# Kernel optimization log

Hardware: AMD Instinct MI355X
Metric: run time of the kernel (lower is better)

## Reference

```python
import jax, jax.numpy as jnp
import numpy as np

N, DIM = 4096, 1024

def setup_inputs() -> dict:
    key = jax.random.key(0)
    ks = jax.random.split(key, 5)
    scale = 1.0 / np.sqrt(DIM)
    return {
        "x": jax.random.normal(ks[0], (N, DIM), dtype=jnp.float32),
        "Wq": jax.random.normal(ks[1], (DIM, DIM), dtype=jnp.float32) * scale,
        "bq": jax.random.normal(ks[2], (DIM,), dtype=jnp.float32) * 0.01,
        "Wk": jax.random.normal(ks[3], (DIM, DIM), dtype=jnp.float32) * scale,
        "bk": jax.random.normal(ks[4], (DIM,), dtype=jnp.float32) * 0.01,
    }

def reference(x, Wq, bq, Wk, bk):
    # torch nn.Linear: y = x @ W.T + b
    q = x @ Wq.T + bq            # [N, D]
    k = x @ Wk.T + bk            # [N, D]
    scores = q @ k.T             # [N, N] (no 1/sqrt(d) scaling, as in source)
    attn = jax.nn.softmax(scores, axis=-1)
    return attn @ x              # weighted pooling over raw x (no value proj)
```

## Files before the change

### kernel.cpp

```cpp
#include <hip/hip_runtime.h>
#include <hip/hip_bf16.h>
#include <hip/hip_fp16.h>
#include <stdint.h>


using half8   = __attribute__((ext_vector_type(8))) _Float16;
using float4v = __attribute__((ext_vector_type(4))) float;
using int4v   = __attribute__((ext_vector_type(4))) int;

#define QS        (6.0f / 32768.0f)
#define INV_S     (32768.0f / 6.0f)
#define INV_S256  (128.0f / 6.0f)
#define C_HH      (65536.0f * QS * QS)
#define C_X       (256.0f * QS * QS)

#define SX        (6.0f / 32768.0f)
#define SW        (0.25f / 32768.0f)
#define P_HH      (65536.0f * SX * SW)
#define P_X       (256.0f * SX * SW)

#define GLOAD_LDS16(gptr, ldsptr)                                              \
  __builtin_amdgcn_global_load_lds(                                            \
      (__attribute__((address_space(1))) void*)(uintptr_t)(gptr),              \
      (__attribute__((address_space(3))) void*)(unsigned)(uintptr_t)(ldsptr),  \
      16, 0, 0)

__global__ __launch_bounds__(256, 2) void gemm_s_stats(
    const int8_t* __restrict__ Ahi, const int8_t* __restrict__ Alo,
    const int8_t* __restrict__ Bhi, const int8_t* __restrict__ Blo,
    _Float16* __restrict__ E, float2* __restrict__ stats)
{
  __shared__ __align__(16) int8_t sAh[128 * 64];
  __shared__ __align__(16) int8_t sAl[128 * 64];
  __shared__ __align__(16) int8_t sBh[128 * 64];
  __shared__ __align__(16) int8_t sBl[128 * 64];

  const int tid  = threadIdx.x;
  const int wave = tid >> 6;
  const int lane = tid & 63;
  const int quad = lane >> 4;
  const int t16  = lane & 15;
  const int wm   = wave & 1;
  const int wn   = wave >> 1;
  const int row0 = blockIdx.y * 128;
  const int col0 = blockIdx.x * 128;

  const int seg  = lane & 3;
  const int rsub = lane >> 2;

  int4v hh[4][4], cc[4][4];
#pragma unroll
  for (int i = 0; i < 4; ++i)
#pragma unroll
    for (int j = 0; j < 4; ++j) {
      hh[i][j] = (int4v){0, 0, 0, 0};
      cc[i][j] = (int4v){0, 0, 0, 0};
    }

  for (int k0 = 0; k0 < 1024; k0 += 64) {
#pragma unroll
    for (int r = 0; r < 2; ++r) {
      const int trow = r * 64 + wave * 16;
      const size_t goffA = (size_t)(row0 + trow + rsub) * 2048 + k0 + seg * 16;
      const size_t goffB = (size_t)(col0 + trow + rsub) * 2048 + k0 + seg * 16;
      GLOAD_LDS16(Ahi + goffA, &sAh[trow * 64]);
      GLOAD_LDS16(Alo + goffA, &sAl[trow * 64]);
      GLOAD_LDS16(Bhi + goffB, &sBh[trow * 64]);
      GLOAD_LDS16(Blo + goffB, &sBl[trow * 64]);
    }
    __syncthreads();

    int4v ah[4], al[4], bh[4], bl[4];
#pragma unroll
    for (int i = 0; i < 4; ++i) {
      const int ar = (wm * 64 + i * 16 + t16) * 64 + quad * 16;
      ah[i] = *(const int4v*)&sAh[ar];
      al[i] = *(const int4v*)&sAl[ar];
    }
#pragma unroll
    for (int j = 0; j < 4; ++j) {
      const int br = (wn * 64 + j * 16 + t16) * 64 + quad * 16;
      bh[j] = *(const int4v*)&sBh[br];
      bl[j] = *(const int4v*)&sBl[br];
    }

#pragma unroll
    for (int i = 0; i < 4; ++i)
#pragma unroll
      for (int j = 0; j < 4; ++j) {
        hh[i][j] = __builtin_amdgcn_mfma_i32_16x16x64_i8(ah[i], bh[j], hh[i][j], 0, 0, 0);
        cc[i][j] = __builtin_amdgcn_mfma_i32_16x16x64_i8(ah[i], bl[j], cc[i][j], 0, 0, 0);
        cc[i][j] = __builtin_amdgcn_mfma_i32_16x16x64_i8(al[i], bh[j], cc[i][j], 0, 0, 0);
      }
    __syncthreads();
  }

  float* red = (float*)sAh;

  float vv[4][4][4];
  float rmax[4][4];
#pragma unroll
  for (int i = 0; i < 4; ++i)
#pragma unroll
    for (int r = 0; r < 4; ++r) {
      float mx = -3.0e38f;
#pragma unroll
      for (int j = 0; j < 4; ++j) {
        float v = C_HH * (float)hh[i][j][r] + C_X * (float)cc[i][j][r];
        vv[i][j][r] = v;
        mx = fmaxf(mx, v);
      }
      mx = fmaxf(mx, __shfl_xor(mx, 1));
      mx = fmaxf(mx, __shfl_xor(mx, 2));
      mx = fmaxf(mx, __shfl_xor(mx, 4));
      mx = fmaxf(mx, __shfl_xor(mx, 8));
      rmax[i][r] = mx;
    }
  if (t16 == 0) {
#pragma unroll
    for (int i = 0; i < 4; ++i)
#pragma unroll
      for (int r = 0; r < 4; ++r)
        red[wn * 128 + wm * 64 + i * 16 + quad * 4 + r] = rmax[i][r];
  }
  __syncthreads();

  float mrow[4][4];
#pragma unroll
  for (int i = 0; i < 4; ++i)
#pragma unroll
    for (int r = 0; r < 4; ++r) {
      const int row = wm * 64 + i * 16 + quad * 4 + r;
      mrow[i][r] = fmaxf(red[row], red[128 + row]);
    }

  float rsum[4][4];
#pragma unroll
  for (int i = 0; i < 4; ++i)
#pragma unroll
    for (int r = 0; r < 4; ++r) {
      float s = 0.f;
#pragma unroll
      for (int j = 0; j < 4; ++j) {
        float e = __expf(vv[i][j][r] - mrow[i][r]);
        vv[i][j][r] = e;
        s += e;
      }
      s += __shfl_xor(s, 1);
      s += __shfl_xor(s, 2);
      s += __shfl_xor(s, 4);
      s += __shfl_xor(s, 8);
      rsum[i][r] = s;
    }
  if (t16 == 0) {
#pragma unroll
    for (int i = 0; i < 4; ++i)
#pragma unroll
      for (int r = 0; r < 4; ++r)
        red[256 + wn * 128 + wm * 64 + i * 16 + quad * 4 + r] = rsum[i][r];
  }
  __syncthreads();

#pragma unroll
  for (int i = 0; i < 4; ++i) {
#pragma unroll
    for (int j = 0; j < 4; ++j) {
#pragma unroll
      for (int r = 0; r < 4; ++r) {
        const int crow = row0 + wm * 64 + i * 16 + quad * 4 + r;
        const int ccol = col0 + wn * 64 + j * 16 + t16;
        E[(size_t)crow * 4096 + ccol] = (_Float16)vv[i][j][r];
      }
    }
  }
  if (wn == 0 && t16 == 0) {
#pragma unroll
    for (int i = 0; i < 4; ++i)
#pragma unroll
      for (int r = 0; r < 4; ++r) {
        const int row = wm * 64 + i * 16 + quad * 4 + r;
        const float l = red[256 + row] + red[256 + 128 + row];
        stats[(size_t)(row0 + row) * 32 + blockIdx.x] =
            make_float2(mrow[i][r], l);
      }
  }
}

__global__ __launch_bounds__(256, 2) void gemm_proj_i8(
    const int8_t* __restrict__ Ahi, const int8_t* __restrict__ Alo,
    const int8_t* __restrict__ Bhi, const int8_t* __restrict__ Blo,
    const float* __restrict__ biasQ, const float* __restrict__ biasK,
    int8_t* __restrict__ Ch, int8_t* __restrict__ Cl)
{
  __shared__ __align__(16) int8_t sAh[128 * 64];
  __shared__ __align__(16) int8_t sAl[128 * 64];
  __shared__ __align__(16) int8_t sBh[128 * 64];
  __shared__ __align__(16) int8_t sBl[128 * 64];

  const int tid  = threadIdx.x;
  const int wave = tid >> 6;
  const int lane = tid & 63;
  const int quad = lane >> 4;
  const int t16  = lane & 15;
  const int wm   = wave & 1;
  const int wn   = wave >> 1;
  const int row0 = blockIdx.y * 128;
  const int col0 = blockIdx.x * 128;

  const int seg  = lane & 3;
  const int rsub = lane >> 2;

  int4v hh[4][4], cc[4][4];
#pragma unroll
  for (int i = 0; i < 4; ++i)
#pragma unroll
    for (int j = 0; j < 4; ++j) {
      hh[i][j] = (int4v){0, 0, 0, 0};
      cc[i][j] = (int4v){0, 0, 0, 0};
    }

  for (int k0 = 0; k0 < 1024; k0 += 64) {
#pragma unroll
    for (int r = 0; r < 2; ++r) {
      const int trow = r * 64 + wave * 16;
      const size_t goffA = (size_t)(row0 + trow + rsub) * 1024 + k0 + seg * 16;
      const size_t goffB = (size_t)(col0 + trow + rsub) * 1024 + k0 + seg * 16;
      GLOAD_LDS16(Ahi + goffA, &sAh[trow * 64]);
      GLOAD_LDS16(Alo + goffA, &sAl[trow * 64]);
      GLOAD_LDS16(Bhi + goffB, &sBh[trow * 64]);
      GLOAD_LDS16(Blo + goffB, &sBl[trow * 64]);
    }
    __syncthreads();

    int4v ah[4], al[4], bh[4], bl[4];
#pragma unroll
    for (int i = 0; i < 4; ++i) {
      const int ar = (wm * 64 + i * 16 + t16) * 64 + quad * 16;
      ah[i] = *(const int4v*)&sAh[ar];
      al[i] = *(const int4v*)&sAl[ar];
    }
#pragma unroll
    for (int j = 0; j < 4; ++j) {
      const int br = (wn * 64 + j * 16 + t16) * 64 + quad * 16;
      bh[j] = *(const int4v*)&sBh[br];
      bl[j] = *(const int4v*)&sBl[br];
    }

#pragma unroll
    for (int i = 0; i < 4; ++i)
#pragma unroll
      for (int j = 0; j < 4; ++j) {
        hh[i][j] = __builtin_amdgcn_mfma_i32_16x16x64_i8(ah[i], bh[j], hh[i][j], 0, 0, 0);
        cc[i][j] = __builtin_amdgcn_mfma_i32_16x16x64_i8(ah[i], bl[j], cc[i][j], 0, 0, 0);
        cc[i][j] = __builtin_amdgcn_mfma_i32_16x16x64_i8(al[i], bh[j], cc[i][j], 0, 0, 0);
      }
    __syncthreads();
  }

#pragma unroll
  for (int i = 0; i < 4; ++i) {
#pragma unroll
    for (int j = 0; j < 4; ++j) {
      const int ccol = col0 + wn * 64 + j * 16 + t16;
      const float* bp = (ccol < 1024) ? biasQ : (biasK - 1024);
#pragma unroll
      for (int r = 0; r < 4; ++r) {
        const int crow = row0 + wm * 64 + i * 16 + quad * 4 + r;
        float v = P_HH * (float)hh[i][j][r] + P_X * (float)cc[i][j][r] + bp[ccol];
        int hi = (int)lrintf(v * INV_S256);
        hi = hi > 127 ? 127 : (hi < -127 ? -127 : hi);
        int lo = (int)lrintf(v * INV_S - 256.0f * (float)hi);
        lo = lo > 127 ? 127 : (lo < -127 ? -127 : lo);
        Ch[(size_t)crow * 2048 + ccol] = (int8_t)hi;
        Cl[(size_t)crow * 2048 + ccol] = (int8_t)lo;
      }
    }
  }
}

__global__ __launch_bounds__(512) void gemm_av(
    const uint16_t* __restrict__ E, const uint16_t* __restrict__ B,
    const float2* __restrict__ stats, float* __restrict__ out)
{
  __shared__ __align__(16) uint16_t stage[16384];
  __shared__ float betaS[128 * 33];

  const int L      = blockIdx.x;
  const int xcd    = L & 7;
  const int rest   = L >> 3;
  const int colb   = rest & 7;
  const int bandHi = rest >> 3;
  const int band   = xcd + 8 * bandHi;
  const int row0   = band * 128;
  const int col0   = colb * 128;

  const int tid  = threadIdx.x;
  const int wave = tid >> 6;
  const int z    = wave >> 2;
  const int gw   = wave & 3;
  const int lane = tid & 63;
  const int quad = lane >> 4;
  const int t16  = lane & 15;
  const int wm   = gw & 1;
  const int wn   = gw >> 1;
  const int seg  = lane & 3;
  const int rsub = lane >> 2;

  if (tid < 128) {
    const int row = row0 + tid;
    float2 st[32];
    float m = -3.0e38f;
#pragma unroll
    for (int t = 0; t < 32; ++t) {
      st[t] = stats[(size_t)row * 32 + t];
      m = fmaxf(m, st[t].x);
    }
    float l = 0.f;
#pragma unroll
    for (int t = 0; t < 32; ++t) l += st[t].y * __expf(st[t].x - m);
    const float inv = 1.0f / l;
#pragma unroll
    for (int t = 0; t < 32; ++t)
      betaS[tid * 33 + t] = __expf(st[t].x - m) * inv;
  }
  __syncthreads();

  uint16_t* sA = &stage[z * 8192];
  uint16_t* sB = &stage[z * 8192 + 4096];

  float4v acc[4][4];
#pragma unroll
  for (int i = 0; i < 4; ++i)
#pragma unroll
    for (int j = 0; j < 4; ++j)
      acc[i][j] = (float4v){0.f, 0.f, 0.f, 0.f};

  for (int tt = 0; tt < 16; ++tt) {
    const int t = z * 16 + tt;
    _Float16 bb[4];
#pragma unroll
    for (int i = 0; i < 4; ++i)
      bb[i] = (_Float16)betaS[(wm * 64 + i * 16 + t16) * 33 + t];

#pragma unroll
    for (int kk = 0; kk < 4; ++kk) {
      const int k0 = t * 128 + kk * 32;
#pragma unroll
      for (int r = 0; r < 2; ++r) {
        const int trow = r * 64 + gw * 16;
        const size_t goffA = (size_t)(row0 + trow + rsub) * 4096 + k0 + seg * 8;
        const size_t goffB = (size_t)(col0 + trow + rsub) * 4096 + k0 + seg * 8;
        GLOAD_LDS16(E + goffA, &sA[trow * 32]);
        GLOAD_LDS16(B + goffB, &sB[trow * 32]);
      }
      __syncthreads();

      half8 af[4], bf[4];
#pragma unroll
      for (int i = 0; i < 4; ++i) {
        af[i] = *(const half8*)&sA[(wm * 64 + i * 16 + t16) * 32 + quad * 8];
        half8 bs;
#pragma unroll
        for (int c = 0; c < 8; ++c) bs[c] = bb[i];
        af[i] = af[i] * bs;
      }
#pragma unroll
      for (int j = 0; j < 4; ++j)
        bf[j] = *(const half8*)&sB[(wn * 64 + j * 16 + t16) * 32 + quad * 8];

#pragma unroll
      for (int i = 0; i < 4; ++i)
#pragma unroll
        for (int j = 0; j < 4; ++j)
          acc[i][j] = __builtin_amdgcn_mfma_f32_16x16x32_f16(af[i], bf[j], acc[i][j], 0, 0, 0);
      __syncthreads();
    }
  }

  float* xfer = (float*)stage;
#pragma unroll
  for (int h = 0; h < 2; ++h) {
    if (z == 1) {
#pragma unroll
      for (int i = 2 * h; i < 2 * h + 2; ++i)
#pragma unroll
        for (int j = 0; j < 4; ++j)
#pragma unroll
          for (int r = 0; r < 4; ++r) {
            const int e = (i - 2 * h) * 16 + j * 4 + r;
            xfer[e * 256 + gw * 64 + lane] = acc[i][j][r];
          }
    }
    __syncthreads();
    if (z == 0) {
#pragma unroll
      for (int i = 2 * h; i < 2 * h + 2; ++i)
#pragma unroll
        for (int j = 0; j < 4; ++j)
#pragma unroll
          for (int r = 0; r < 4; ++r) {
            const int e = (i - 2 * h) * 16 + j * 4 + r;
            acc[i][j][r] += xfer[e * 256 + gw * 64 + lane];
          }
    }
    __syncthreads();
  }

  if (z == 0) {
#pragma unroll
    for (int i = 0; i < 4; ++i) {
#pragma unroll
      for (int j = 0; j < 4; ++j) {
        const int ccol = col0 + wn * 64 + j * 16 + t16;
#pragma unroll
        for (int r = 0; r < 4; ++r) {
          const int crow = row0 + wm * 64 + i * 16 + quad * 4 + r;
          out[(size_t)crow * 1024 + ccol] = acc[i][j][r];
        }
      }
    }
  }
}

__global__ __launch_bounds__(256) void quantT(
    const float* __restrict__ x, const float* __restrict__ Wq,
    const float* __restrict__ Wk,
    int8_t* __restrict__ xhi, int8_t* __restrict__ xlo,
    int8_t* __restrict__ whi, int8_t* __restrict__ wlo,
    uint16_t* __restrict__ xT)
{
  if (blockIdx.x < 6144) {
    int i = blockIdx.x * 256 + threadIdx.x;
    const float* src; int8_t* dh; int8_t* dl; int idx; float s256, s;
    if (i < 1048576)      { src = x;  idx = i;           dh = xhi; dl = xlo;
                            s256 = INV_S256; s = INV_S; }
    else if (i < 1310720) { src = Wq; idx = i - 1048576; dh = whi; dl = wlo;
                            s256 = 512.0f; s = 131072.0f; }
    else                  { src = Wk; idx = i - 1310720; dh = whi + 1048576;
                            dl = wlo + 1048576; s256 = 512.0f; s = 131072.0f; }
    float4 v = ((const float4*)src)[idx];
    float vv[4] = {v.x, v.y, v.z, v.w};
    int hp = 0, lp = 0;
#pragma unroll
    for (int c = 0; c < 4; ++c) {
      int h = (int)lrintf(vv[c] * s256);
      h = h > 127 ? 127 : (h < -127 ? -127 : h);
      int l = (int)lrintf(vv[c] * s - 256.0f * (float)h);
      l = l > 127 ? 127 : (l < -127 ? -127 : l);
      hp |= (h & 0xff) << (8 * c);
      lp |= (l & 0xff) << (8 * c);
    }
    ((int*)dh)[idx] = hp;
    ((int*)dl)[idx] = lp;
  } else {
    __shared__ float tile[32][33];
    const int tb = blockIdx.x - 6144;
    const int bx = tb & 31;
    const int by = tb >> 5;
    const int tx = threadIdx.x & 31;
    const int ty = threadIdx.x >> 5;
#pragma unroll
    for (int p = 0; p < 4; ++p) {
      const int row = by * 32 + ty + p * 8;
      tile[ty + p * 8][tx] = x[(size_t)row * 1024 + bx * 32 + tx];
    }
    __syncthreads();
#pragma unroll
    for (int p = 0; p < 4; ++p) {
      const int oc = ty + p * 8;
      __half hv = __float2half_rn(tile[tx][oc]);
      xT[(size_t)(bx * 32 + oc) * 4096 + by * 32 + tx] = *(uint16_t*)&hv;
    }
  }
}

extern "C" void kernel_launch(void* const* d_in, const int* in_sizes, int n_in,
                              void* d_out, int out_size, void* d_ws, size_t ws_size,
                              hipStream_t stream) {
  const int N = 4096, D = 1024;
  const float* x  = (const float*)d_in[0];
  const float* Wq = (const float*)d_in[1];
  const float* bq = (const float*)d_in[2];
  const float* Wk = (const float*)d_in[3];
  const float* bk = (const float*)d_in[4];
  float* out = (float*)d_out;

  char* w = (char*)d_ws;
  const size_t MiB = 1024 * 1024;
  int8_t*    xq_hi  = (int8_t*)   (w + 0  * MiB);
  int8_t*    xq_lo  = (int8_t*)   (w + 4  * MiB);
  int8_t*    Wqk_hi = (int8_t*)   (w + 8  * MiB);
  int8_t*    Wqk_lo = (int8_t*)   (w + 10 * MiB);
  int8_t*    qk_hi  = (int8_t*)   (w + 12 * MiB);
  int8_t*    qk_lo  = (int8_t*)   (w + 20 * MiB);
  _Float16*  E      = (_Float16*) (w + 36 * MiB);
  float2*    stats  = (float2*)   (w + 68 * MiB);
  uint16_t*  xTh    = (uint16_t*) (w + 72 * MiB);

  quantT<<<10240, 256, 0, stream>>>(x, Wq, Wk, xq_hi, xq_lo, Wqk_hi, Wqk_lo,
                                    xTh);

  gemm_proj_i8<<<dim3(2048 / 128, N / 128), 256, 0, stream>>>(
      xq_hi, xq_lo, Wqk_hi, Wqk_lo, bq, bk, qk_hi, qk_lo);

  gemm_s_stats<<<dim3(N / 128, N / 128), 256, 0, stream>>>(
      qk_hi, qk_lo, qk_hi + 1024, qk_lo + 1024, E, stats);

  gemm_av<<<256, 512, 0, stream>>>((const uint16_t*)E, xTh, stats, out);

  (void)in_sizes; (void)n_in; (void)out_size; (void)ws_size;
}
```

Before: 243.8 us.

## Double-buffer LDS with async prefetch and XOR-swizzle tiles in all three GEMMs

Converts the three GEMM kernels to double-buffered LDS staging. The next K-slice is issued via global_load_lds before the current slice is computed, with explicit vmcnt waits and raw barriers replacing __syncthreads. It also XOR-swizzles the 16-byte chunk placement per row to reduce LDS bank conflicts on the fragment reads. The cost is doubled LDS use, which may cut occupancy (the int8 kernels go to 64KB per block with launch_bounds 2), and the hand-written vmcnt counts must match the number of loads issued.

Result: faster. 221.8 us (-9.0%).

```diff
diff --git a/kernel.cpp b/kernel.cpp
--- a/kernel.cpp
+++ b/kernel.cpp
@@ -25,15 +25,21 @@
       (__attribute__((address_space(3))) void*)(unsigned)(uintptr_t)(ldsptr),  \
       16, 0, 0)
 
+__device__ __forceinline__ void barrier_raw() {
+  asm volatile("" ::: "memory");
+  __builtin_amdgcn_s_barrier();
+  asm volatile("" ::: "memory");
+}
+
 __global__ __launch_bounds__(256, 2) void gemm_s_stats(
     const int8_t* __restrict__ Ahi, const int8_t* __restrict__ Alo,
     const int8_t* __restrict__ Bhi, const int8_t* __restrict__ Blo,
     _Float16* __restrict__ E, float2* __restrict__ stats)
 {
-  __shared__ __align__(16) int8_t sAh[128 * 64];
-  __shared__ __align__(16) int8_t sAl[128 * 64];
-  __shared__ __align__(16) int8_t sBh[128 * 64];
-  __shared__ __align__(16) int8_t sBl[128 * 64];
+  __shared__ __align__(16) int8_t sAh[2][128 * 64];
+  __shared__ __align__(16) int8_t sAl[2][128 * 64];
+  __shared__ __align__(16) int8_t sBh[2][128 * 64];
+  __shared__ __align__(16) int8_t sBl[2][128 * 64];
 
   const int tid  = threadIdx.x;
   const int wave = tid >> 6;
@@ -47,6 +53,8 @@
 
   const int seg  = lane & 3;
   const int rsub = lane >> 2;
+  const int segS = seg ^ (rsub & 3);
+  const int rch  = (quad ^ (t16 & 3)) * 16;
 
   int4v hh[4][4], cc[4][4];
 #pragma unroll
@@ -57,31 +65,43 @@
       cc[i][j] = (int4v){0, 0, 0, 0};
     }
 
-  for (int k0 = 0; k0 < 1024; k0 += 64) {
+  auto stage_k = [&](int ks, int b) {
+    const int k0 = ks * 64;
 #pragma unroll
     for (int r = 0; r < 2; ++r) {
       const int trow = r * 64 + wave * 16;
-      const size_t goffA = (size_t)(row0 + trow + rsub) * 2048 + k0 + seg * 16;
-      const size_t goffB = (size_t)(col0 + trow + rsub) * 2048 + k0 + seg * 16;
-      GLOAD_LDS16(Ahi + goffA, &sAh[trow * 64]);
-      GLOAD_LDS16(Alo + goffA, &sAl[trow * 64]);
-      GLOAD_LDS16(Bhi + goffB, &sBh[trow * 64]);
-      GLOAD_LDS16(Blo + goffB, &sBl[trow * 64]);
-    }
-    __syncthreads();
+      const size_t goffA = (size_t)(row0 + trow + rsub) * 2048 + k0 + segS * 16;
+      const size_t goffB = (size_t)(col0 + trow + rsub) * 2048 + k0 + segS * 16;
+      GLOAD_LDS16(Ahi + goffA, &sAh[b][trow * 64]);
+      GLOAD_LDS16(Alo + goffA, &sAl[b][trow * 64]);
+      GLOAD_LDS16(Bhi + goffB, &sBh[b][trow * 64]);
+      GLOAD_LDS16(Blo + goffB, &sBl[b][trow * 64]);
+    }
+  };
+
+  stage_k(0, 0);
+  int buf = 0;
+  for (int ks = 0; ks < 16; ++ks) {
+    if (ks < 15) {
+      stage_k(ks + 1, buf ^ 1);
+      asm volatile("s_waitcnt vmcnt(8)" ::: "memory");
+    } else {
+      asm volatile("s_waitcnt vmcnt(0)" ::: "memory");
+    }
+    barrier_raw();
 
     int4v ah[4], al[4], bh[4], bl[4];
 #pragma unroll
     for (int i = 0; i < 4; ++i) {
-      const int ar = (wm * 64 + i * 16 + t16) * 64 + quad * 16;
-      ah[i] = *(const int4v*)&sAh[ar];
-      al[i] = *(const int4v*)&sAl[ar];
+      const int ao = (wm * 64 + i * 16 + t16) * 64 + rch;
+      ah[i] = *(const int4v*)&sAh[buf][ao];
+      al[i] = *(const int4v*)&sAl[buf][ao];
     }
 #pragma unroll
     for (int j = 0; j < 4; ++j) {
-      const int br = (wn * 64 + j * 16 + t16) * 64 + quad * 16;
-      bh[j] = *(const int4v*)&sBh[br];
-      bl[j] = *(const int4v*)&sBl[br];
+      const int bo = (wn * 64 + j * 16 + t16) * 64 + rch;
+      bh[j] = *(const int4v*)&sBh[buf][bo];
+      bl[j] = *(const int4v*)&sBl[buf][bo];
     }
 
 #pragma unroll
@@ -92,7 +112,8 @@
         cc[i][j] = __builtin_amdgcn_mfma_i32_16x16x64_i8(ah[i], bl[j], cc[i][j], 0, 0, 0);
         cc[i][j] = __builtin_amdgcn_mfma_i32_16x16x64_i8(al[i], bh[j], cc[i][j], 0, 0, 0);
       }
-    __syncthreads();
+    barrier_raw();
+    buf ^= 1;
   }
 
   float* red = (float*)sAh;
@@ -192,10 +213,10 @@
     const float* __restrict__ biasQ, const float* __restrict__ biasK,
     int8_t* __restrict__ Ch, int8_t* __restrict__ Cl)
 {
-  __shared__ __align__(16) int8_t sAh[128 * 64];
-  __shared__ __align__(16) int8_t sAl[128 * 64];
-  __shared__ __align__(16) int8_t sBh[128 * 64];
-  __shared__ __align__(16) int8_t sBl[128 * 64];
+  __shared__ __align__(16) int8_t sAh[2][128 * 64];
+  __shared__ __align__(16) int8_t sAl[2][128 * 64];
+  __shared__ __align__(16) int8_t sBh[2][128 * 64];
+  __shared__ __align__(16) int8_t sBl[2][128 * 64];
 
   const int tid  = threadIdx.x;
   const int wave = tid >> 6;
@@ -209,6 +230,8 @@
 
   const int seg  = lane & 3;
   const int rsub = lane >> 2;
+  const int segS = seg ^ (rsub & 3);
+  const int rch  = (quad ^ (t16 & 3)) * 16;
 
   int4v hh[4][4], cc[4][4];
 #pragma unroll
@@ -219,31 +242,43 @@
       cc[i][j] = (int4v){0, 0, 0, 0};
     }
 
-  for (int k0 = 0; k0 < 1024; k0 += 64) {
+  auto stage_k = [&](int ks, int b) {
+    const int k0 = ks * 64;
 #pragma unroll
     for (int r = 0; r < 2; ++r) {
       const int trow = r * 64 + wave * 16;
-      const size_t goffA = (size_t)(row0 + trow + rsub) * 1024 + k0 + seg * 16;
-      const size_t goffB = (size_t)(col0 + trow + rsub) * 1024 + k0 + seg * 16;
-      GLOAD_LDS16(Ahi + goffA, &sAh[trow * 64]);
-      GLOAD_LDS16(Alo + goffA, &sAl[trow * 64]);
-      GLOAD_LDS16(Bhi + goffB, &sBh[trow * 64]);
-      GLOAD_LDS16(Blo + goffB, &sBl[trow * 64]);
-    }
-    __syncthreads();
+      const size_t goffA = (size_t)(row0 + trow + rsub) * 1024 + k0 + segS * 16;
+      const size_t goffB = (size_t)(col0 + trow + rsub) * 1024 + k0 + segS * 16;
+      GLOAD_LDS16(Ahi + goffA, &sAh[b][trow * 64]);
+      GLOAD_LDS16(Alo + goffA, &sAl[b][trow * 64]);
+      GLOAD_LDS16(Bhi + goffB, &sBh[b][trow * 64]);
+      GLOAD_LDS16(Blo + goffB, &sBl[b][trow * 64]);
+    }
+  };
+
+  stage_k(0, 0);
+  int buf = 0;
+  for (int ks = 0; ks < 16; ++ks) {
+    if (ks < 15) {
+      stage_k(ks + 1, buf ^ 1);
+      asm volatile("s_waitcnt vmcnt(8)" ::: "memory");
+    } else {
+      asm volatile("s_waitcnt vmcnt(0)" ::: "memory");
+    }
+    barrier_raw();
 
     int4v ah[4], al[4], bh[4], bl[4];
 #pragma unroll
     for (int i = 0; i < 4; ++i) {
-      const int ar = (wm * 64 + i * 16 + t16) * 64 + quad * 16;
-      ah[i] = *(const int4v*)&sAh[ar];
-      al[i] = *(const int4v*)&sAl[ar];
+      const int ao = (wm * 64 + i * 16 + t16) * 64 + rch;
+      ah[i] = *(const int4v*)&sAh[buf][ao];
+      al[i] = *(const int4v*)&sAl[buf][ao];
     }
 #pragma unroll
     for (int j = 0; j < 4; ++j) {
-      const int br = (wn * 64 + j * 16 + t16) * 64 + quad * 16;
-      bh[j] = *(const int4v*)&sBh[br];
-      bl[j] = *(const int4v*)&sBl[br];
+      const int bo = (wn * 64 + j * 16 + t16) * 64 + rch;
+      bh[j] = *(const int4v*)&sBh[buf][bo];
+      bl[j] = *(const int4v*)&sBl[buf][bo];
     }
 
 #pragma unroll
@@ -254,7 +289,8 @@
         cc[i][j] = __builtin_amdgcn_mfma_i32_16x16x64_i8(ah[i], bl[j], cc[i][j], 0, 0, 0);
         cc[i][j] = __builtin_amdgcn_mfma_i32_16x16x64_i8(al[i], bh[j], cc[i][j], 0, 0, 0);
       }
-    __syncthreads();
+    barrier_raw();
+    buf ^= 1;
   }
 
 #pragma unroll
@@ -282,7 +318,7 @@
     const uint16_t* __restrict__ E, const uint16_t* __restrict__ B,
     const float2* __restrict__ stats, float* __restrict__ out)
 {
-  __shared__ __align__(16) uint16_t stage[16384];
+  __shared__ __align__(16) uint16_t stage[2][16384];
   __shared__ float betaS[128 * 33];
 
   const int L      = blockIdx.x;
@@ -305,6 +341,8 @@
   const int wn   = gw >> 1;
   const int seg  = lane & 3;
   const int rsub = lane >> 2;
+  const int segS = seg ^ (rsub & 3);
+  const int rch8 = (quad ^ (t16 & 3)) * 8;
 
   if (tid < 128) {
     const int row = row0 + tid;
@@ -325,9 +363,6 @@
   }
   __syncthreads();
 
-  uint16_t* sA = &stage[z * 8192];
-  uint16_t* sB = &stage[z * 8192 + 4096];
-
   float4v acc[4][4];
 #pragma unroll
   for (int i = 0; i < 4; ++i)
@@ -335,46 +370,61 @@
     for (int j = 0; j < 4; ++j)
       acc[i][j] = (float4v){0.f, 0.f, 0.f, 0.f};
 
-  for (int tt = 0; tt < 16; ++tt) {
-    const int t = z * 16 + tt;
+  auto stage_s = [&](int s, int b) {
+    const int k0 = (z * 16 + (s >> 2)) * 128 + (s & 3) * 32;
+    uint16_t* sA = &stage[b][z * 8192];
+    uint16_t* sB = &stage[b][z * 8192 + 4096];
+#pragma unroll
+    for (int r = 0; r < 2; ++r) {
+      const int trow = r * 64 + gw * 16;
+      const size_t goffA = (size_t)(row0 + trow + rsub) * 4096 + k0 + segS * 8;
+      const size_t goffB = (size_t)(col0 + trow + rsub) * 4096 + k0 + segS * 8;
+      GLOAD_LDS16(E + goffA, &sA[trow * 32]);
+      GLOAD_LDS16(B + goffB, &sB[trow * 32]);
+    }
+  };
+
+  stage_s(0, 0);
+  int buf = 0;
+  for (int s = 0; s < 64; ++s) {
+    if (s < 63) {
+      stage_s(s + 1, buf ^ 1);
+      asm volatile("s_waitcnt vmcnt(4)" ::: "memory");
+    } else {
+      asm volatile("s_waitcnt vmcnt(0)" ::: "memory");
+    }
+    barrier_raw();
+
+    const int t = z * 16 + (s >> 2);
     _Float16 bb[4];
 #pragma unroll
     for (int i = 0; i < 4; ++i)
       bb[i] = (_Float16)betaS[(wm * 64 + i * 16 + t16) * 33 + t];
 
-#pragma unroll
-    for (int kk = 0; kk < 4; ++kk) {
-      const int k0 = t * 128 + kk * 32;
-#pragma unroll
-      for (int r = 0; r < 2; ++r) {
-        const int trow = r * 64 + gw * 16;
-        const size_t goffA = (size_t)(row0 + trow + rsub) * 4096 + k0 + seg * 8;
-        const size_t goffB = (size_t)(col0 + trow + rsub) * 4096 + k0 + seg * 8;
-        GLOAD_LDS16(E + goffA, &sA[trow * 32]);
-        GLOAD_LDS16(B + goffB, &sB[trow * 32]);
-      }
-      __syncthreads();
-
-      half8 af[4], bf[4];
-#pragma unroll
-      for (int i = 0; i < 4; ++i) {
-        af[i] = *(const half8*)&sA[(wm * 64 + i * 16 + t16) * 32 + quad * 8];
-        half8 bs;
-#pragma unroll
-        for (int c = 0; c < 8; ++c) bs[c] = bb[i];
-        af[i] = af[i] * bs;
-      }
+    const uint16_t* sA = &stage[buf][z * 8192];
+    const uint16_t* sB = &stage[buf][z * 8192 + 4096];
+
+    half8 af[4], bf[4];
+#pragma unroll
+    for (int i = 0; i < 4; ++i) {
+      af[i] = *(const half8*)&sA[(wm * 64 + i * 16 + t16) * 32 + rch8];
+      half8 bs;
+#pragma unroll
+      for (int c = 0; c < 8; ++c) bs[c] = bb[i];
+      af[i] = af[i] * bs;
+    }
+#pragma unroll
+    for (int j = 0; j < 4; ++j)
+      bf[j] = *(const half8*)&sB[(wn * 64 + j * 16 + t16) * 32 + rch8];
+
+#pragma unroll
+    for (int i = 0; i < 4; ++i)
 #pragma unroll
       for (int j = 0; j < 4; ++j)
-        bf[j] = *(const half8*)&sB[(wn * 64 + j * 16 + t16) * 32 + quad * 8];
-
-#pragma unroll
-      for (int i = 0; i < 4; ++i)
-#pragma unroll
-        for (int j = 0; j < 4; ++j)
-          acc[i][j] = __builtin_amdgcn_mfma_f32_16x16x32_f16(af[i], bf[j], acc[i][j], 0, 0, 0);
-      __syncthreads();
-    }
+        acc[i][j] = __builtin_amdgcn_mfma_f32_16x16x32_f16(af[i], bf[j], acc[i][j], 0, 0, 0);
+
+    barrier_raw();
+    buf ^= 1;
   }
 
   float* xfer = (float*)stage;
```
